# Performance work log

Measured on AMD Instinct MI355X. Metric: run time of the kernel, lower is better.

## Reference

```python
import jax, jax.numpy as jnp
import numpy as np

N = 10000      # atoms
E = 320000     # edges (avg degree 32)
C = 128        # hidden_channels
NB = 32        # num_basis
L = 3          # num_layers
CUT = 5.0      # cutoff
G = 8          # graphs in batch


def setup_inputs() -> dict:
    key = jax.random.key(0)
    ks = jax.random.split(key, 32)
    pos = jax.random.normal(ks[0], (N, 3), dtype=jnp.float32) * 2.0
    z = jax.random.randint(ks[1], (N,), 0, 100)
    row = jax.random.randint(ks[2], (E,), 0, N)
    # avoid self-loops so edge_length > 0
    col = (row + 1 + jax.random.randint(ks[3], (E,), 0, N - 1)) % N
    edge_index = jnp.stack([row, col])
    shifts = jnp.zeros((E, 3), dtype=jnp.float32)
    batch_index = jnp.sort(jax.random.randint(ks[4], (N,), 0, G))
    s = 0.05
    p = lambda k, shape: jax.random.normal(k, shape, dtype=jnp.float32) * s
    return {
        'z': z, 'pos': pos, 'edge_index': edge_index, 'shifts': shifts,
        'batch_index': batch_index,
        'emb': p(ks[5], (100, C)),
        # message blocks (stacked over layers)
        'm_w1': p(ks[6], (L, C, C)), 'm_b1': p(ks[7], (L, C)),
        'm_w2': p(ks[8], (L, C, 3 * C)), 'm_b2': p(ks[9], (L, 3 * C)),
        'f_w': p(ks[10], (L, NB, 3 * C)), 'f_b': p(ks[11], (L, 3 * C)),
        # update blocks
        'u_w': p(ks[12], (L, C, C)), 'v_w': p(ks[13], (L, C, C)),
        'up_w1': p(ks[14], (L, 2 * C, C)), 'up_b1': p(ks[15], (L, C)),
        'up_w2': p(ks[16], (L, C, 3 * C)), 'up_b2': p(ks[17], (L, 3 * C)),
        # readout
        'r_w1': p(ks[18], (C, C // 2)), 'r_b1': p(ks[19], (C // 2,)),
        'r_w2': p(ks[20], (C // 2, 1)), 'r_b2': p(ks[21], (1,)),
    }


def painn_energy(pos, shifts, emb, m_w1, m_b1, m_w2, m_b2, f_w, f_b,
                 u_w, v_w, up_w1, up_b1, up_w2, up_b2,
                 r_w1, r_b1, r_w2, r_b2, z, edge_index, batch_index):
    row, col = edge_index[0], edge_index[1]
    scalar = emb[z]                                  # [N, C]
    vector = jnp.zeros((N, 3, C), dtype=pos.dtype)   # [N, 3, C]

    edge_vec = pos[col] - pos[row] + shifts          # [E, 3]
    edge_len = jnp.sqrt(jnp.sum(edge_vec * edge_vec, axis=-1) + 1e-12)  # [E]
    direction = edge_vec / edge_len[:, None]

    # smooth bump envelope (C-inf, compact support)
    scaled = edge_len / CUT
    inside = scaled < 1.0
    denom = jnp.where(inside, 1.0 - scaled * scaled, 1.0)
    gate = jnp.where(inside, jnp.exp(1.0 - 1.0 / denom), 0.0)  # [E]

    # gaussian radial basis
    centers = jnp.linspace(0.0, CUT, NB)
    gamma = 1.0 / (centers[1] - centers[0]) ** 2
    rbf = jnp.exp(-gamma * (edge_len[:, None] - centers) ** 2)  # [E, NB]
    edge_attr = rbf * gate[:, None]

    for l in range(L):
        # --- message ---
        h = jax.nn.silu(scalar[col] @ m_w1[l] + m_b1[l]) @ m_w2[l] + m_b2[l]  # [E, 3C]
        w = h * (edge_attr @ f_w[l] + f_b[l]) * gate[:, None]
        w1, w2, w3 = jnp.split(w, 3, axis=-1)                                 # each [E, C]
        d_scalar = jax.ops.segment_sum(w1, row, num_segments=N)
        msg_vec = vector[col] * w2[:, None, :] + w3[:, None, :] * direction[:, :, None]  # [E,3,C]
        d_vector = jax.ops.segment_sum(msg_vec, row, num_segments=N)
        scalar = scalar + d_scalar
        vector = vector + d_vector
        # --- update ---
        uv = vector @ u_w[l]                                   # [N, 3, C]
        vv = vector @ v_w[l]
        v_norm = jnp.sqrt(jnp.sum(vv * vv, axis=1) + 1e-8)     # [N, C]
        a = jax.nn.silu(jnp.concatenate([scalar, v_norm], axis=-1) @ up_w1[l] + up_b1[l]) @ up_w2[l] + up_b2[l]
        a1, a2, a3 = jnp.split(a, 3, axis=-1)
        scalar = scalar + a1 + a2 * jnp.sum(uv * vv, axis=1)
        vector = vector + a3[:, None, :] * uv

    e_atom = jax.nn.silu(scalar @ r_w1 + r_b1) @ r_w2 + r_b2   # [N, 1]
    return jax.ops.segment_sum(e_atom, batch_index, num_segments=G)  # [G, 1]


def reference(z, pos, edge_index, shifts, batch_index, emb,
              m_w1, m_b1, m_w2, m_b2, f_w, f_b,
              u_w, v_w, up_w1, up_b1, up_w2, up_b2,
              r_w1, r_b1, r_w2, r_b2):
    return painn_energy(pos, shifts, emb, m_w1, m_b1, m_w2, m_b2, f_w, f_b,
                        u_w, v_w, up_w1, up_b1, up_w2, up_b2,
                        r_w1, r_b1, r_w2, r_b2, z, edge_index, batch_index)
```

## Files before the change

kernel.cpp:

```cpp
#include <hip/hip_runtime.h>
#include <math.h>

#define CUTR 5.0f
#define TL 2048
#define NBASIS 32
#define HSC 16.0f
#define TSC 16.0f
#define VSC 64.0f
#define INV_HT (1.0f / (HSC * TSC))
#define INV_HTV (1.0f / (HSC * TSC * VSC))

typedef __attribute__((ext_vector_type(8))) short bf16x8;
typedef __attribute__((ext_vector_type(4))) float f32x4;
typedef __attribute__((ext_vector_type(2))) float f32x2;

struct U3 { uint x, y, z; };
struct U2 { uint x, y; };

__device__ __forceinline__ float silu_f(float x) { return x / (1.0f + expf(-x)); }
__device__ __forceinline__ ushort f2bf(float x) {
  uint b = __float_as_uint(x);
  uint r = (b + 0x7FFFu + ((b >> 16) & 1u)) >> 16;
  return (ushort)r;
}
__device__ __forceinline__ float bf2f(ushort u) { return __uint_as_float((uint)u << 16); }
__device__ __forceinline__ uchar f2fp8(float x) {
  return (uchar)(__builtin_amdgcn_cvt_pk_fp8_f32(x, 0.0f, 0, false) & 0xff);
}
__device__ __forceinline__ f32x2 fp8lo(uint u) {
  return __builtin_amdgcn_cvt_pk_f32_fp8((int)u, false);
}
__device__ __forceinline__ f32x2 fp8hi(uint u) {
  return __builtin_amdgcn_cvt_pk_f32_fp8((int)u, true);
}

__global__ __launch_bounds__(384) void table_kernel(const float* __restrict__ f_w,
                                                    const float* __restrict__ f_b,
                                                    uchar* __restrict__ tab) {
  __shared__ float fws[NBASIS * 384];
  __shared__ float rbf[8][NBASIS];
  __shared__ float gv[8];
  int tid = threadIdx.x;
  int bi = blockIdx.x;
  int l = bi >> 8, tb = bi & 255;
  for (int i = tid; i < NBASIS * 384; i += 384) fws[i] = f_w[l * NBASIS * 384 + i];
  if (tid < 256) {
    int tt = tid >> 5, k = tid & 31;
    float len = (float)(tb * 8 + tt) * (CUTR / (float)(TL - 1));
    const float gamma = (31.0f / 5.0f) * (31.0f / 5.0f);
    float c = 5.0f * (float)k / 31.0f;
    float d = len - c;
    rbf[tt][k] = expf(-gamma * d * d);
    if (k == 0) {
      float s = len * (1.0f / CUTR);
      gv[tt] = (s < 1.0f) ? expf(1.0f - 1.0f / (1.0f - s * s)) : 0.0f;
    }
  }
  __syncthreads();
  int j = tid % 384;
  int b = j >> 7, ch = j & 127;
  float fb = f_b[l * 384 + j];
  for (int tt = 0; tt < 8; ++tt) {
    float acc = 0.0f;
#pragma unroll
    for (int k = 0; k < NBASIS; ++k) acc += rbf[tt][k] * fws[k * 384 + j];
    float g = gv[tt];
    tab[((size_t)l * TL + (size_t)(tb * 8 + tt)) * 512 + (ch >> 1) * 8 + b * 2 + (ch & 1)] =
        f2fp8(g * (g * acc + fb) * TSC);
  }
}

__global__ __launch_bounds__(256) void init_kernel(
    const int* __restrict__ z, const float* __restrict__ emb, float* __restrict__ scalar,
    ushort* __restrict__ sbf, const float* __restrict__ m_w1, const float* __restrict__ m_w2,
    const float* __restrict__ u_w, const float* __restrict__ v_w,
    const float* __restrict__ up_w1, const float* __restrict__ up_w2,
    const float* __restrict__ r_w1, ushort* __restrict__ wt, const float* __restrict__ pos,
    const int* __restrict__ ei, const float* __restrict__ shifts, int* __restrict__ counts,
    int N, int E) {
  int tid = threadIdx.x;
  int bi = blockIdx.x;
  int nbEmb = (N * 128 + 255) / 256;
  int nbW = (548864 + 255) / 256;
  if (bi < nbEmb) {
    int idx = bi * 256 + tid;
    if (idx >= N * 128) return;
    int n = idx >> 7, j = idx & 127;
    float v = emb[z[n] * 128 + j];
    scalar[idx] = v;
    sbf[idx] = f2bf(v);
    return;
  }
  bi -= nbEmb;
  if (bi < nbW) {
    int idx = bi * 256 + tid;
    if (idx >= 548864) return;
    float v;
    if (idx >= 540672) {
      int t = idx - 540672;
      int n = t >> 7, k = t & 127;
      v = r_w1[k * 64 + n];
    } else {
      int l = idx / 180224, local = idx % 180224;
      if (local < 16384) {
        int n = local >> 7, k = local & 127;
        v = m_w1[l * 16384 + k * 128 + n];
      } else if (local < 65536) {
        int t = local - 16384;
        int n = t >> 7, k = t & 127;
        v = m_w2[l * 49152 + k * 384 + n];
      } else if (local < 98304) {
        int t = local - 65536;
        int n = t >> 7, k = t & 127;
        v = (n < 128) ? u_w[l * 16384 + k * 128 + n] : v_w[l * 16384 + k * 128 + (n - 128)];
      } else if (local < 131072) {
        int t = local - 98304;
        int n = t >> 8, k = t & 255;
        v = up_w1[l * 32768 + k * 128 + n];
      } else {
        int t = local - 131072;
        int n = t >> 7, k = t & 127;
        v = up_w2[l * 49152 + k * 384 + n];
      }
    }
    wt[idx] = f2bf(v);
    return;
  }
  bi -= nbW;
  {
    int e = bi * 256 + tid;
    if (e >= E) return;
    int r = ei[e], c = ei[E + e];
    float dx = pos[c * 3 + 0] - pos[r * 3 + 0] + shifts[e * 3 + 0];
    float dy = pos[c * 3 + 1] - pos[r * 3 + 1] + shifts[e * 3 + 1];
    float dz = pos[c * 3 + 2] - pos[r * 3 + 2] + shifts[e * 3 + 2];
    float len = sqrtf(dx * dx + dy * dy + dz * dz + 1e-12f);
    if (len < CUTR) atomicAdd(&counts[r], 1);
  }
}

__global__ __launch_bounds__(1024) void scan_kernel(const int* __restrict__ counts,
                                                    int* __restrict__ offs,
                                                    int* __restrict__ cursor, int N) {
  __shared__ int sm[1024];
  int tid = threadIdx.x;
  int CH = (N + 1023) / 1024;
  int base = tid * CH;
  int sum = 0;
  for (int i = 0; i < CH; i++) sum += (base + i < N) ? counts[base + i] : 0;
  sm[tid] = sum;
  __syncthreads();
  for (int o = 1; o < 1024; o <<= 1) {
    int v = (tid >= o) ? sm[tid - o] : 0;
    __syncthreads();
    sm[tid] += v;
    __syncthreads();
  }
  int run = sm[tid] - sum;
  for (int i = 0; i < CH; i++) {
    if (base + i < N) {
      offs[base + i] = run;
      cursor[base + i] = run;
      run += counts[base + i];
    }
  }
  if (tid == 1023) offs[N] = sm[1023];
}

__global__ void fill_kernel(const float* __restrict__ pos, const int* __restrict__ ei,
                            const float* __restrict__ shifts, int* __restrict__ cursor,
                            float4* __restrict__ pk, int E) {
  int e = blockIdx.x * 256 + threadIdx.x;
  if (e >= E) return;
  int r = ei[e], c = ei[E + e];
  float dx = pos[c * 3 + 0] - pos[r * 3 + 0] + shifts[e * 3 + 0];
  float dy = pos[c * 3 + 1] - pos[r * 3 + 1] + shifts[e * 3 + 1];
  float dz = pos[c * 3 + 2] - pos[r * 3 + 2] + shifts[e * 3 + 2];
  float len = sqrtf(dx * dx + dy * dy + dz * dz + 1e-12f);
  if (len >= CUTR) return;
  float inv = 1.0f / len;
  float x = len * ((float)(TL - 1) / CUTR);
  int ib = (int)(x + 0.5f);
  if (ib > TL - 1) ib = TL - 1;
  int p = atomicAdd(&cursor[r], 1);
  pk[p] = make_float4(__int_as_float(c | (ib << 14)), dx * inv, dy * inv, dz * inv);
}

template <bool FIRST>
__global__ __launch_bounds__(256) void message_kernel(
    const int* __restrict__ offs, const float4* __restrict__ pk, const uchar* __restrict__ hv8,
    const uchar* __restrict__ tab8, float* __restrict__ scalar, ushort* __restrict__ sbf,
    float* __restrict__ vec, ushort* __restrict__ vbout, int N) {
  int lane = threadIdx.x & 63;
  int n = blockIdx.x * 4 + (threadIdx.x >> 6);
  if (n >= N) return;
  int p0 = offs[n], p1 = offs[n + 1];
  float aS0 = 0.f, aS1 = 0.f;
  float aW00 = 0.f, aW01 = 0.f, aW10 = 0.f, aW11 = 0.f, aW20 = 0.f, aW21 = 0.f;
  float aD00 = 0.f, aD01 = 0.f, aD10 = 0.f, aD11 = 0.f, aD20 = 0.f, aD21 = 0.f;
  int p = p0;
  bool hasA = p < p1, hasB = p + 1 < p1;
  float4 cA, cB;
  if (hasA) cA = pk[p];
  if (hasB) cB = pk[p + 1];
  while (hasA) {
    int bitsA = __float_as_int(cA.x);
    int colA = bitsA & 16383, ibA = bitsA >> 14;
    U3 hvA;
    if (FIRST) {
      U2 t = *(const U2*)(hv8 + (size_t)colA * 768 + lane * 12);
      hvA.x = t.x; hvA.y = t.y; hvA.z = 0;
    } else {
      hvA = *(const U3*)(hv8 + (size_t)colA * 768 + lane * 12);
    }
    U2 tA = *(const U2*)(tab8 + (size_t)ibA * 512 + lane * 8);
    U3 hvB;
    U2 tB;
    float4 dB;
    if (hasB) {
      int bitsB = __float_as_int(cB.x);
      int colB = bitsB & 16383, ibB = bitsB >> 14;
      dB = cB;
      if (FIRST) {
        U2 t = *(const U2*)(hv8 + (size_t)colB * 768 + lane * 12);
        hvB.x = t.x; hvB.y = t.y; hvB.z = 0;
      } else {
        hvB = *(const U3*)(hv8 + (size_t)colB * 768 + lane * 12);
      }
      tB = *(const U2*)(tab8 + (size_t)ibB * 512 + lane * 8);
    }
    int pn = p + 2;
    bool nA = pn < p1, nB = pn + 1 < p1;
    float4 fA, fB;
    if (nA) fA = pk[pn];
    if (nB) fB = pk[pn + 1];
    {
      f32x2 h1 = fp8lo(hvA.x), h2 = fp8hi(hvA.x);
      f32x2 h3 = fp8lo(hvA.y);
      f32x2 t1 = fp8lo(tA.x), t2 = fp8hi(tA.x), t3 = fp8lo(tA.y);
      aS0 += h1.x * t1.x;
      aS1 += h1.y * t1.y;
      float w3l = h3.x * t3.x, w3h = h3.y * t3.y;
      if (!FIRST) {
        f32x2 v0 = fp8hi(hvA.y), v1 = fp8lo(hvA.z), v2 = fp8hi(hvA.z);
        float w2l = h2.x * t2.x, w2h = h2.y * t2.y;
        aW00 += v0.x * w2l; aW01 += v0.y * w2h;
        aW10 += v1.x * w2l; aW11 += v1.y * w2h;
        aW20 += v2.x * w2l; aW21 += v2.y * w2h;
      }
      aD00 += w3l * cA.y; aD01 += w3h * cA.y;
      aD10 += w3l * cA.z; aD11 += w3h * cA.z;
      aD20 += w3l * cA.w; aD21 += w3h * cA.w;
    }
    if (hasB) {
      f32x2 h1 = fp8lo(hvB.x), h2 = fp8hi(hvB.x);
      f32x2 h3 = fp8lo(hvB.y);
      f32x2 t1 = fp8lo(tB.x), t2 = fp8hi(tB.x), t3 = fp8lo(tB.y);
      aS0 += h1.x * t1.x;
      aS1 += h1.y * t1.y;
      float w3l = h3.x * t3.x, w3h = h3.y * t3.y;
      if (!FIRST) {
        f32x2 v0 = fp8hi(hvB.y), v1 = fp8lo(hvB.z), v2 = fp8hi(hvB.z);
        float w2l = h2.x * t2.x, w2h = h2.y * t2.y;
        aW00 += v0.x * w2l; aW01 += v0.y * w2h;
        aW10 += v1.x * w2l; aW11 += v1.y * w2h;
        aW20 += v2.x * w2l; aW21 += v2.y * w2h;
      }
      aD00 += w3l * dB.y; aD01 += w3h * dB.y;
      aD10 += w3l * dB.z; aD11 += w3h * dB.z;
      aD20 += w3l * dB.w; aD21 += w3h * dB.w;
    }
    cA = fA;
    cB = fB;
    hasA = nA;
    hasB = nB;
    p = pn;
  }
  float sS0 = aS0 * INV_HT, sS1 = aS1 * INV_HT;
  float sV00 = aD00 * INV_HT, sV01 = aD01 * INV_HT;
  float sV10 = aD10 * INV_HT, sV11 = aD11 * INV_HT;
  float sV20 = aD20 * INV_HT, sV21 = aD21 * INV_HT;
  if (!FIRST) {
    sV00 += aW00 * INV_HTV; sV01 += aW01 * INV_HTV;
    sV10 += aW10 * INV_HTV; sV11 += aW11 * INV_HTV;
    sV20 += aW20 * INV_HTV; sV21 += aW21 * INV_HTV;
  }
  float2* sp = (float2*)(scalar + (size_t)n * 128) + lane;
  float2 sv = *sp;
  sv.x += sS0;
  sv.y += sS1;
  *sp = sv;
  ((uint*)(sbf + (size_t)n * 128))[lane] = (uint)f2bf(sv.x) | ((uint)f2bf(sv.y) << 16);
  float2* vp0 = (float2*)(vec + (size_t)n * 384) + lane;
  float2* vp1 = (float2*)(vec + (size_t)n * 384 + 128) + lane;
  float2* vp2 = (float2*)(vec + (size_t)n * 384 + 256) + lane;
  float2 v0, v1, v2;
  if (FIRST) {
    v0 = make_float2(sV00, sV01);
    v1 = make_float2(sV10, sV11);
    v2 = make_float2(sV20, sV21);
  } else {
    v0 = *vp0; v1 = *vp1; v2 = *vp2;
    v0.x += sV00; v0.y += sV01;
    v1.x += sV10; v1.y += sV11;
    v2.x += sV20; v2.y += sV21;
  }
  *vp0 = v0; *vp1 = v1; *vp2 = v2;
  uint* ob = (uint*)(vbout + (size_t)n * 384);
  ob[lane] = (uint)f2bf(v0.x) | ((uint)f2bf(v0.y) << 16);
  ob[lane + 64] = (uint)f2bf(v1.x) | ((uint)f2bf(v1.y) << 16);
  ob[lane + 128] = (uint)f2bf(v2.x) | ((uint)f2bf(v2.y) << 16);
}

__global__ __launch_bounds__(512) void mlp_kernel(const ushort* __restrict__ A,
                                                  const ushort* __restrict__ W1T,
                                                  const float* __restrict__ b1,
                                                  const ushort* __restrict__ W2T,
                                                  const float* __restrict__ b2,
                                                  uchar* __restrict__ out, int M) {
  __shared__ ushort As[32 * 128];
  __shared__ ushort Bs[128 * 128];
  __shared__ ushort Hs[32 * 128];
  int tid = threadIdx.x;
  int lane = tid & 63, w = tid >> 6;
  int mh = w >> 2, wc = w & 3;
  int m0 = blockIdx.x * 32;
  int cl = lane & 15, rq = lane >> 4;
  int ra = mh * 16 + cl;
  f32x4 acc[2] = {};
  {
    {
      int row = tid >> 4, ch = tid & 15;
      uint4 av = make_uint4(0, 0, 0, 0);
      if (m0 + row < M) av = *(const uint4*)(A + (size_t)(m0 + row) * 128 + ch * 8);
      *(uint4*)(&As[row * 128 + ((ch ^ (row & 7)) * 8)]) = av;
    }
#pragma unroll
    for (int r = 0; r < 4; ++r) {
      int c = tid + r * 512;
      int row = c >> 4, ch = c & 15;
      uint4 bv = *(const uint4*)(W1T + (size_t)row * 128 + ch * 8);
      *(uint4*)(&Bs[row * 128 + ((ch ^ (row & 7)) * 8)]) = bv;
    }
    __syncthreads();
#pragma unroll
    for (int ks = 0; ks < 4; ++ks) {
      int ch = ks * 4 + rq;
      bf16x8 a = *(bf16x8*)&As[ra * 128 + ((ch ^ (ra & 7)) * 8)];
#pragma unroll
      for (int ns = 0; ns < 2; ++ns) {
        int rb = wc * 32 + ns * 16 + cl;
        bf16x8 b = *(bf16x8*)&Bs[rb * 128 + ((ch ^ (rb & 7)) * 8)];
        acc[ns] = __builtin_amdgcn_mfma_f32_16x16x32_bf16(a, b, acc[ns], 0, 0, 0);
      }
    }
  }
#pragma unroll
  for (int ns = 0; ns < 2; ++ns) {
    int hcol = wc * 32 + ns * 16 + cl;
    float bv = b1[hcol];
    int chunk = hcol >> 3, el = hcol & 7;
#pragma unroll
    for (int j = 0; j < 4; ++j) {
      int hr = mh * 16 + rq * 4 + j;
      float v = silu_f(acc[ns][j] + bv);
      Hs[hr * 128 + ((chunk ^ (hr & 7)) * 8) + el] = f2bf(v);
    }
  }
  __syncthreads();
  for (int nt = 0; nt < 3; ++nt) {
#pragma unroll
    for (int r = 0; r < 4; ++r) {
      int c = tid + r * 512;
      int row = c >> 4, ch = c & 15;
      uint4 bv = *(const uint4*)(W2T + (size_t)(nt * 128 + row) * 128 + ch * 8);
      *(uint4*)(&Bs[row * 128 + ((ch ^ (row & 7)) * 8)]) = bv;
    }
    __syncthreads();
    f32x4 acc2[2] = {};
#pragma unroll
    for (int ks = 0; ks < 4; ++ks) {
      int ch = ks * 4 + rq;
      bf16x8 a = *(bf16x8*)&Hs[ra * 128 + ((ch ^ (ra & 7)) * 8)];
#pragma unroll
      for (int ns = 0; ns < 2; ++ns) {
        int rb = wc * 32 + ns * 16 + cl;
        bf16x8 b = *(bf16x8*)&Bs[rb * 128 + ((ch ^ (rb & 7)) * 8)];
        acc2[ns] = __builtin_amdgcn_mfma_f32_16x16x32_bf16(a, b, acc2[ns], 0, 0, 0);
      }
    }
#pragma unroll
    for (int ns = 0; ns < 2; ++ns) {
      int ch = wc * 32 + ns * 16 + cl;
      float bv = b2[nt * 128 + ch];
#pragma unroll
      for (int j = 0; j < 4; ++j) {
        int m = m0 + mh * 16 + rq * 4 + j;
        if (m >= M) continue;
        out[(size_t)m * 768 + (ch >> 1) * 12 + nt * 2 + (ch & 1)] =
            f2fp8((acc2[ns][j] + bv) * HSC);
      }
    }
    __syncthreads();
  }
}

template <bool LAST>
__global__ __launch_bounds__(512) void mlp2_kernel(
    const ushort* __restrict__ sbf_in, const ushort* __restrict__ W1T,
    const float* __restrict__ b1, const ushort* __restrict__ W2T, const float* __restrict__ b2,
    const ushort* __restrict__ uvvv, float* __restrict__ scalar, ushort* __restrict__ sbf,
    float* __restrict__ vec, uchar* __restrict__ hv8, const ushort* __restrict__ W1nT,
    const float* __restrict__ b1n, const ushort* __restrict__ W2nT,
    const float* __restrict__ b2n, int M) {
  __shared__ ushort As[16 * 128];
  __shared__ ushort Bs[128 * 128];
  __shared__ ushort Hs[16 * 128];
  int tid = threadIdx.x;
  int lane = tid & 63, w = tid >> 6;
  int m0 = blockIdx.x * 16;
  int cl = lane & 15, rq = lane >> 4;
  int rb = w * 16 + cl;
  f32x4 acc = {};
  for (int k0 = 0; k0 < 256; k0 += 128) {
    __syncthreads();
    if (tid < 256) {
      int row = tid >> 4, ch = tid & 15;
      uint4 av = make_uint4(0, 0, 0, 0);
      if (m0 + row < M) {
        if (k0 == 0) {
          av = *(const uint4*)(sbf_in + (size_t)(m0 + row) * 128 + ch * 8);
        } else {
          const ushort* ub = uvvv + (size_t)(m0 + row) * 768 + 128 + ch * 8;
          bf16x8 x0 = *(const bf16x8*)(ub);
          bf16x8 x1 = *(const bf16x8*)(ub + 256);
          bf16x8 x2 = *(const bf16x8*)(ub + 512);
          ushort pkv[8];
#pragma unroll
          for (int e = 0; e < 8; ++e) {
            float a = bf2f((ushort)x0[e]), bb = bf2f((ushort)x1[e]), cc = bf2f((ushort)x2[e]);
            pkv[e] = f2bf(sqrtf(a * a + bb * bb + cc * cc + 1e-8f));
          }
          av = *(uint4*)pkv;
        }
      }
      *(uint4*)(&As[row * 128 + ((ch ^ (row & 7)) * 8)]) = av;
    }
#pragma unroll
    for (int r = 0; r < 4; ++r) {
      int c = tid + r * 512;
      int row = c >> 4, ch = c & 15;
      uint4 bv = *(const uint4*)(W1T + (size_t)row * 256 + k0 + ch * 8);
      *(uint4*)(&Bs[row * 128 + ((ch ^ (row & 7)) * 8)]) = bv;
    }
    __syncthreads();
#pragma unroll
    for (int ks = 0; ks < 4; ++ks) {
      int ch = ks * 4 + rq;
      bf16x8 a = *(bf16x8*)&As[cl * 128 + ((ch ^ (cl & 7)) * 8)];
      bf16x8 b = *(bf16x8*)&Bs[rb * 128 + ((ch ^ (rb & 7)) * 8)];
      acc = __builtin_amdgcn_mfma_f32_16x16x32_bf16(a, b, acc, 0, 0, 0);
    }
  }
  {
    int hcol = w * 16 + cl;
    float bv = b1[hcol];
    int chunk = hcol >> 3, el = hcol & 7;
#pragma unroll
    for (int j = 0; j < 4; ++j) {
      int hr = rq * 4 + j;
      Hs[hr * 128 + ((chunk ^ (hr & 7)) * 8) + el] = f2bf(silu_f(acc[j] + bv));
    }
  }
  __syncthreads();
  f32x4 aReg[3];
  for (int nt = 0; nt < 3; ++nt) {
#pragma unroll
    for (int r = 0; r < 4; ++r) {
      int c = tid + r * 512;
      int row = c >> 4, ch = c & 15;
      uint4 bv = *(const uint4*)(W2T + (size_t)(nt * 128 + row) * 128 + ch * 8);
      *(uint4*)(&Bs[row * 128 + ((ch ^ (row & 7)) * 8)]) = bv;
    }
    __syncthreads();
    f32x4 acc2 = {};
#pragma unroll
    for (int ks = 0; ks < 4; ++ks) {
      int ch = ks * 4 + rq;
      bf16x8 a = *(bf16x8*)&Hs[cl * 128 + ((ch ^ (cl & 7)) * 8)];
      bf16x8 b = *(bf16x8*)&Bs[rb * 128 + ((ch ^ (rb & 7)) * 8)];
      acc2 = __builtin_amdgcn_mfma_f32_16x16x32_bf16(a, b, acc2, 0, 0, 0);
    }
    aReg[nt] = acc2;
    __syncthreads();
  }
  {
    int chOff = w * 16 + cl;
    float b2a = b2[chOff], b2b = b2[128 + chOff], b2c = b2[256 + chOff];
#pragma unroll
    for (int j = 0; j < 4; ++j) {
      int nn = m0 + rq * 4 + j;
      if (nn >= M) continue;
      float a1 = aReg[0][j] + b2a;
      float a2 = aReg[1][j] + b2b;
      float a3 = aReg[2][j] + b2c;
      const ushort* ub = uvvv + (size_t)nn * 768;
      float uv0 = bf2f(ub[chOff]), vv0 = bf2f(ub[128 + chOff]);
      float uv1 = bf2f(ub[256 + chOff]), vv1 = bf2f(ub[384 + chOff]);
      float uv2 = bf2f(ub[512 + chOff]), vv2 = bf2f(ub[640 + chOff]);
      float dot = uv0 * vv0 + uv1 * vv1 + uv2 * vv2;
      size_t si = (size_t)nn * 128 + chOff;
      float s = scalar[si] + a1 + a2 * dot;
      scalar[si] = s;
      ushort sb = f2bf(s);
      sbf[si] = sb;
      if (!LAST) {
        int lr = rq * 4 + j;
        As[lr * 128 + (((chOff >> 3) ^ (lr & 7)) * 8) + (chOff & 7)] = sb;
        size_t vb = (size_t)nn * 384 + chOff;
        float nv0 = vec[vb] + a3 * uv0;
        float nv1 = vec[vb + 128] + a3 * uv1;
        float nv2 = vec[vb + 256] + a3 * uv2;
        vec[vb] = nv0;
        vec[vb + 128] = nv1;
        vec[vb + 256] = nv2;
        size_t hb = (size_t)nn * 768 + (chOff >> 1) * 12 + 6 + (chOff & 1);
        hv8[hb] = f2fp8(nv0 * VSC);
        hv8[hb + 2] = f2fp8(nv1 * VSC);
        hv8[hb + 4] = f2fp8(nv2 * VSC);
      }
    }
  }
  if (LAST) return;
#pragma unroll
  for (int r = 0; r < 4; ++r) {
    int c = tid + r * 512;
    int row = c >> 4, ch = c & 15;
    uint4 bv = *(const uint4*)(W1nT + (size_t)row * 128 + ch * 8);
    *(uint4*)(&Bs[row * 128 + ((ch ^ (row & 7)) * 8)]) = bv;
  }
  __syncthreads();
  f32x4 acc3 = {};
#pragma unroll
  for (int ks = 0; ks < 4; ++ks) {
    int ch = ks * 4 + rq;
    bf16x8 a = *(bf16x8*)&As[cl * 128 + ((ch ^ (cl & 7)) * 8)];
    bf16x8 b = *(bf16x8*)&Bs[rb * 128 + ((ch ^ (rb & 7)) * 8)];
    acc3 = __builtin_amdgcn_mfma_f32_16x16x32_bf16(a, b, acc3, 0, 0, 0);
  }
  __syncthreads();
  {
    int hcol = w * 16 + cl;
    float bv = b1n[hcol];
    int chunk = hcol >> 3, el = hcol & 7;
#pragma unroll
    for (int j = 0; j < 4; ++j) {
      int hr = rq * 4 + j;
      Hs[hr * 128 + ((chunk ^ (hr & 7)) * 8) + el] = f2bf(silu_f(acc3[j] + bv));
    }
  }
  __syncthreads();
  for (int nt = 0; nt < 3; ++nt) {
#pragma unroll
    for (int r = 0; r < 4; ++r) {
      int c = tid + r * 512;
      int row = c >> 4, ch = c & 15;
      uint4 bv = *(const uint4*)(W2nT + (size_t)(nt * 128 + row) * 128 + ch * 8);
      *(uint4*)(&Bs[row * 128 + ((ch ^ (row & 7)) * 8)]) = bv;
    }
    __syncthreads();
    f32x4 acc4 = {};
#pragma unroll
    for (int ks = 0; ks < 4; ++ks) {
      int ch = ks * 4 + rq;
      bf16x8 a = *(bf16x8*)&Hs[cl * 128 + ((ch ^ (cl & 7)) * 8)];
      bf16x8 b = *(bf16x8*)&Bs[rb * 128 + ((ch ^ (rb & 7)) * 8)];
      acc4 = __builtin_amdgcn_mfma_f32_16x16x32_bf16(a, b, acc4, 0, 0, 0);
    }
    {
      int ch = w * 16 + cl;
      float bv = b2n[nt * 128 + ch];
#pragma unroll
      for (int j = 0; j < 4; ++j) {
        int m = m0 + rq * 4 + j;
        if (m >= M) continue;
        hv8[(size_t)m * 768 + (ch >> 1) * 12 + nt * 2 + (ch & 1)] =
            f2fp8((acc4[j] + bv) * HSC);
      }
    }
    __syncthreads();
  }
}

__global__ __launch_bounds__(256) void gemm_kernel(const ushort* __restrict__ A,
                                                   const ushort* __restrict__ WT,
                                                   ushort* __restrict__ Cout, int M, int K,
                                                   int Nn) {
  __shared__ ushort As[64 * 128];
  __shared__ ushort Bs[64 * 128];
  int tid = threadIdx.x;
  int m0 = blockIdx.x * 64, n0 = blockIdx.y * 64;
  int lane = tid & 63, w = tid >> 6, wr = w >> 1, wc = w & 1;
  f32x4 acc[2][2] = {};
  for (int k0 = 0; k0 < K; k0 += 128) {
    __syncthreads();
#pragma unroll
    for (int r = 0; r < 4; ++r) {
      int c = tid + r * 256;
      int row = c >> 4, col16 = c & 15;
      uint4 av = make_uint4(0, 0, 0, 0);
      if (m0 + row < M) av = *(const uint4*)(A + (size_t)(m0 + row) * K + k0 + col16 * 8);
      *(uint4*)(&As[row * 128 + ((col16 ^ (row & 7)) * 8)]) = av;
      uint4 bv = *(const uint4*)(WT + (size_t)(n0 + row) * K + k0 + col16 * 8);
      *(uint4*)(&Bs[row * 128 + ((col16 ^ (row & 7)) * 8)]) = bv;
    }
    __syncthreads();
#pragma unroll
    for (int ks = 0; ks < 4; ++ks) {
      int ch = ks * 4 + (lane >> 4);
      int ra0 = wr * 32 + (lane & 15), ra1 = ra0 + 16;
      int rb0 = wc * 32 + (lane & 15), rb1 = rb0 + 16;
      bf16x8 a0 = *(bf16x8*)&As[ra0 * 128 + ((ch ^ (ra0 & 7)) * 8)];
      bf16x8 a1 = *(bf16x8*)&As[ra1 * 128 + ((ch ^ (ra1 & 7)) * 8)];
      bf16x8 b0 = *(bf16x8*)&Bs[rb0 * 128 + ((ch ^ (rb0 & 7)) * 8)];
      bf16x8 b1 = *(bf16x8*)&Bs[rb1 * 128 + ((ch ^ (rb1 & 7)) * 8)];
      acc[0][0] = __builtin_amdgcn_mfma_f32_16x16x32_bf16(a0, b0, acc[0][0], 0, 0, 0);
      acc[0][1] = __builtin_amdgcn_mfma_f32_16x16x32_bf16(a0, b1, acc[0][1], 0, 0, 0);
      acc[1][0] = __builtin_amdgcn_mfma_f32_16x16x32_bf16(a1, b0, acc[1][0], 0, 0, 0);
      acc[1][1] = __builtin_amdgcn_mfma_f32_16x16x32_bf16(a1, b1, acc[1][1], 0, 0, 0);
    }
  }
  int cl = lane & 15, rq = lane >> 4;
#pragma unroll
  for (int ms = 0; ms < 2; ++ms)
#pragma unroll
    for (int ns = 0; ns < 2; ++ns) {
      int n = n0 + wc * 32 + ns * 16 + cl;
#pragma unroll
      for (int j = 0; j < 4; ++j) {
        int m = m0 + wr * 32 + ms * 16 + rq * 4 + j;
        if (m >= M) continue;
        Cout[(size_t)m * Nn + n] = f2bf(acc[ms][ns][j]);
      }
    }
}

__global__ __launch_bounds__(256) void readout_kernel(
    const ushort* __restrict__ sbf, const ushort* __restrict__ r1T, const float* __restrict__ rb1,
    const float* __restrict__ r_w2, const float* __restrict__ r_b2, const int* __restrict__ bidx,
    float* __restrict__ out, int N, int G) {
  __shared__ ushort As[64 * 128];
  __shared__ ushort Bs[64 * 128];
  __shared__ float rs[64];
  __shared__ float sm[64];
  int tid = threadIdx.x;
  int m0 = blockIdx.x * 64;
  int lane = tid & 63, w = tid >> 6, wr = w >> 1, wc = w & 1;
  int cl = lane & 15, rq = lane >> 4;
#pragma unroll
  for (int r = 0; r < 4; ++r) {
    int c = tid + r * 256;
    int row = c >> 4, ch = c & 15;
    uint4 av = make_uint4(0, 0, 0, 0);
    if (m0 + row < N) av = *(const uint4*)(sbf + (size_t)(m0 + row) * 128 + ch * 8);
    *(uint4*)(&As[row * 128 + ((ch ^ (row & 7)) * 8)]) = av;
    uint4 bv = *(const uint4*)(r1T + (size_t)row * 128 + ch * 8);
    *(uint4*)(&Bs[row * 128 + ((ch ^ (row & 7)) * 8)]) = bv;
  }
  if (tid < 64) {
    rs[tid] = 0.f;
    sm[tid] = 0.f;
  }
  __syncthreads();
  f32x4 acc[2][2] = {};
#pragma unroll
  for (int ks = 0; ks < 4; ++ks) {
    int ch = ks * 4 + rq;
    int ra0 = wr * 32 + cl, ra1 = ra0 + 16;
    int rb0 = wc * 32 + cl, rb1 = rb0 + 16;
    bf16x8 a0 = *(bf16x8*)&As[ra0 * 128 + ((ch ^ (ra0 & 7)) * 8)];
    bf16x8 a1 = *(bf16x8*)&As[ra1 * 128 + ((ch ^ (ra1 & 7)) * 8)];
    bf16x8 b0 = *(bf16x8*)&Bs[rb0 * 128 + ((ch ^ (rb0 & 7)) * 8)];
    bf16x8 b1 = *(bf16x8*)&Bs[rb1 * 128 + ((ch ^ (rb1 & 7)) * 8)];
    acc[0][0] = __builtin_amdgcn_mfma_f32_16x16x32_bf16(a0, b0, acc[0][0], 0, 0, 0);
    acc[0][1] = __builtin_amdgcn_mfma_f32_16x16x32_bf16(a0, b1, acc[0][1], 0, 0, 0);
    acc[1][0] = __builtin_amdgcn_mfma_f32_16x16x32_bf16(a1, b0, acc[1][0], 0, 0, 0);
    acc[1][1] = __builtin_amdgcn_mfma_f32_16x16x32_bf16(a1, b1, acc[1][1], 0, 0, 0);
  }
#pragma unroll
  for (int ms = 0; ms < 2; ++ms) {
    float part0 = 0.f, part1 = 0.f, part2 = 0.f, part3 = 0.f;
#pragma unroll
    for (int ns = 0; ns < 2; ++ns) {
      int col = wc * 32 + ns * 16 + cl;
      float b1v = rb1[col], wv = r_w2[col];
      part0 += silu_f(acc[ms][ns][0] + b1v) * wv;
      part1 += silu_f(acc[ms][ns][1] + b1v) * wv;
      part2 += silu_f(acc[ms][ns][2] + b1v) * wv;
      part3 += silu_f(acc[ms][ns][3] + b1v) * wv;
    }
#pragma unroll
    for (int o = 1; o < 16; o <<= 1) {
      part0 += __shfl_xor(part0, o);
      part1 += __shfl_xor(part1, o);
      part2 += __shfl_xor(part2, o);
      part3 += __shfl_xor(part3, o);
    }
    if (cl == 0) {
      int rbase = wr * 32 + ms * 16 + rq * 4;
      atomicAdd(&rs[rbase + 0], part0);
      atomicAdd(&rs[rbase + 1], part1);
      atomicAdd(&rs[rbase + 2], part2);
      atomicAdd(&rs[rbase + 3], part3);
    }
  }
  __syncthreads();
  float rb2 = r_b2[0];
  if (tid < 64) {
    int m = m0 + tid;
    if (m < N) atomicAdd(&sm[bidx[m]], rs[tid] + rb2);
  }
  __syncthreads();
  if (tid < G && G <= 64) atomicAdd(&out[tid], sm[tid]);
}

extern "C" void kernel_launch(void* const* d_in, const int* in_sizes, int n_in, void* d_out,
                              int out_size, void* d_ws, size_t ws_size, hipStream_t stream) {
  const int N = in_sizes[0];
  const int E = in_sizes[2] / 2;
  const int G = out_size;

  const int* z = (const int*)d_in[0];
  const float* pos = (const float*)d_in[1];
  const int* ei = (const int*)d_in[2];
  const float* shifts = (const float*)d_in[3];
  const int* bidx = (const int*)d_in[4];
  const float* emb = (const float*)d_in[5];
  const float* m_w1 = (const float*)d_in[6];
  const float* m_b1 = (const float*)d_in[7];
  const float* m_w2 = (const float*)d_in[8];
  const float* m_b2 = (const float*)d_in[9];
  const float* f_w = (const float*)d_in[10];
  const float* f_b = (const float*)d_in[11];
  const float* u_w = (const float*)d_in[12];
  const float* v_w = (const float*)d_in[13];
  const float* up_w1 = (const float*)d_in[14];
  const float* up_b1 = (const float*)d_in[15];
  const float* up_w2 = (const float*)d_in[16];
  const float* up_b2 = (const float*)d_in[17];
  const float* r_w1 = (const float*)d_in[18];
  const float* r_b1 = (const float*)d_in[19];
  const float* r_w2 = (const float*)d_in[20];
  const float* r_b2 = (const float*)d_in[21];
  float* out = (float*)d_out;

  float* w = (float*)d_ws;
  size_t off = 0;
  auto alloc = [&](size_t nfl) { float* p = w + off; off += (nfl + 3) & ~(size_t)3; return p; };
  uchar* tab8 = (uchar*)alloc((size_t)3 * TL * 128);
  float* scalar = alloc((size_t)N * 128);
  ushort* sbf = (ushort*)alloc((size_t)N * 64);
  float* vec = alloc((size_t)N * 384);
  uchar* hv8 = (uchar*)alloc((size_t)N * 192);
  ushort* mir_bf = (ushort*)alloc((size_t)N * 192);
  ushort* uvvv = (ushort*)alloc((size_t)N * 384);
  float* pkf = alloc((size_t)E * 4);
  ushort* wt = (ushort*)alloc((size_t)274432);
  int* counts = (int*)alloc((size_t)N);
  int* offs = (int*)alloc((size_t)N + 4);
  int* cursor = (int*)alloc((size_t)N);
  if (off * sizeof(float) > ws_size) return;

  hipMemsetAsync(counts, 0, (size_t)N * sizeof(int), stream);
  hipMemsetAsync(out, 0, (size_t)G * sizeof(float), stream);

  table_kernel<<<3 * (TL / 8), 384, 0, stream>>>(f_w, f_b, tab8);
  int nbEmb = (N * 128 + 255) / 256;
  int nbW = (548864 + 255) / 256;
  int nbCount = (E + 255) / 256;
  init_kernel<<<nbEmb + nbW + nbCount, 256, 0, stream>>>(z, emb, scalar, sbf, m_w1, m_w2, u_w,
                                                         v_w, up_w1, up_w2, r_w1, wt, pos, ei,
                                                         shifts, counts, N, E);
  scan_kernel<<<1, 1024, 0, stream>>>(counts, offs, cursor, N);
  fill_kernel<<<(E + 255) / 256, 256, 0, stream>>>(pos, ei, shifts, cursor, (float4*)pkf, E);

  dim3 gm((N + 31) / 32);
  dim3 gm2((N + 15) / 16);
  dim3 g3((3 * N + 63) / 64, 4);

  mlp_kernel<<<gm, 512, 0, stream>>>(sbf, wt, m_b1, wt + 16384, m_b2, hv8, N);

  for (int l = 0; l < 3; l++) {
    const ushort* wl = wt + (size_t)l * 180224;
    if (l == 0)
      message_kernel<true><<<(N + 3) / 4, 256, 0, stream>>>(
          offs, (const float4*)pkf, hv8, tab8 + (size_t)l * TL * 512, scalar, sbf, vec, mir_bf,
          N);
    else
      message_kernel<false><<<(N + 3) / 4, 256, 0, stream>>>(
          offs, (const float4*)pkf, hv8, tab8 + (size_t)l * TL * 512, scalar, sbf, vec, mir_bf,
          N);
    gemm_kernel<<<g3, 256, 0, stream>>>(mir_bf, wl + 65536, uvvv, 3 * N, 128, 256);
    if (l < 2) {
      const ushort* wn = wt + (size_t)(l + 1) * 180224;
      mlp2_kernel<false><<<gm2, 512, 0, stream>>>(
          sbf, wl + 98304, up_b1 + l * 128, wl + 131072, up_b2 + l * 384, uvvv, scalar, sbf, vec,
          hv8, wn, m_b1 + (l + 1) * 128, wn + 16384, m_b2 + (l + 1) * 384, N);
    } else {
      mlp2_kernel<true><<<gm2, 512, 0, stream>>>(
          sbf, wl + 98304, up_b1 + l * 128, wl + 131072, up_b2 + l * 384, uvvv, scalar, sbf, vec,
          hv8, wt, m_b1, wt, m_b2, N);
    }
  }

  readout_kernel<<<(N + 63) / 64, 256, 0, stream>>>(sbf, wt + 540672, r_b1, r_w2, r_b2, bidx,
                                                    out, N, G);
}
```

Before: 305.5 us.

## Prepack MLP weights in MFMA fragment order and read directly from global

Adds a pre-pass in init_kernel that converts the update-MLP and next-layer message-MLP weights into a bf16 layout matching the per-lane MFMA B-fragment order. mlp2_kernel then loads B fragments straight from global or L2 instead of staging 128x128 weight tiles through shared memory. This removes the large Bs buffer and most __syncthreads, which cuts LDS use and may raise occupancy. In exchange every 16-row block re-reads the full weights from cache, and the A operand is now built in registers per lane.

```diff
diff --git a/kernel.cpp b/kernel.cpp
--- a/kernel.cpp
+++ b/kernel.cpp
@@ -75,13 +75,14 @@
     ushort* __restrict__ sbf, const float* __restrict__ m_w1, const float* __restrict__ m_w2,
     const float* __restrict__ u_w, const float* __restrict__ v_w,
     const float* __restrict__ up_w1, const float* __restrict__ up_w2,
-    const float* __restrict__ r_w1, ushort* __restrict__ wt, const float* __restrict__ pos,
-    const int* __restrict__ ei, const float* __restrict__ shifts, int* __restrict__ counts,
-    int N, int E) {
+    const float* __restrict__ r_w1, ushort* __restrict__ wt, ushort* __restrict__ wp,
+    const float* __restrict__ pos, const int* __restrict__ ei, const float* __restrict__ shifts,
+    int* __restrict__ counts, int N, int E) {
   int tid = threadIdx.x;
   int bi = blockIdx.x;
   int nbEmb = (N * 128 + 255) / 256;
   int nbW = (548864 + 255) / 256;
+  int nbP = (442368 + 255) / 256;
   if (bi < nbEmb) {
     int idx = bi * 256 + tid;
     if (idx >= N * 128) return;
@@ -127,6 +128,47 @@
     return;
   }
   bi -= nbW;
+  if (bi < nbP) {
+    int idx = bi * 256 + tid;
+    if (idx >= 442368) return;
+    int l = idx / 147456, loc = idx % 147456;
+    float v;
+    if (loc < 32768) {
+      int fid = loc >> 9, li = loc & 511;
+      int ctg = fid >> 3, f = fid & 7;
+      int lane = li >> 3, e = li & 7;
+      int col = ctg * 16 + (lane & 15);
+      int k = (f * 4 + (lane >> 4)) * 8 + e;
+      v = up_w1[l * 32768 + k * 128 + col];
+    } else if (loc < 81920) {
+      int t = loc - 32768;
+      int fid = t >> 9, li = t & 511;
+      int ctg = fid >> 2, f = fid & 3;
+      int lane = li >> 3, e = li & 7;
+      int col = ctg * 16 + (lane & 15);
+      int k = (f * 4 + (lane >> 4)) * 8 + e;
+      v = up_w2[l * 49152 + k * 384 + col];
+    } else if (loc < 98304) {
+      int t = loc - 81920;
+      int fid = t >> 9, li = t & 511;
+      int ctg = fid >> 2, f = fid & 3;
+      int lane = li >> 3, e = li & 7;
+      int col = ctg * 16 + (lane & 15);
+      int k = (f * 4 + (lane >> 4)) * 8 + e;
+      v = m_w1[l * 16384 + k * 128 + col];
+    } else {
+      int t = loc - 98304;
+      int fid = t >> 9, li = t & 511;
+      int ctg = fid >> 2, f = fid & 3;
+      int lane = li >> 3, e = li & 7;
+      int col = ctg * 16 + (lane & 15);
+      int k = (f * 4 + (lane >> 4)) * 8 + e;
+      v = m_w2[l * 49152 + k * 384 + col];
+    }
+    wp[idx] = f2bf(v);
+    return;
+  }
+  bi -= nbP;
   {
     int e = bi * 256 + tid;
     if (e >= E) return;
@@ -407,60 +449,45 @@
 
 template <bool LAST>
 __global__ __launch_bounds__(512) void mlp2_kernel(
-    const ushort* __restrict__ sbf_in, const ushort* __restrict__ W1T,
-    const float* __restrict__ b1, const ushort* __restrict__ W2T, const float* __restrict__ b2,
+    const ushort* __restrict__ sbf_in, const ushort* __restrict__ p_w1,
+    const float* __restrict__ b1, const ushort* __restrict__ p_w2, const float* __restrict__ b2,
     const ushort* __restrict__ uvvv, float* __restrict__ scalar, ushort* __restrict__ sbf,
-    float* __restrict__ vec, uchar* __restrict__ hv8, const ushort* __restrict__ W1nT,
-    const float* __restrict__ b1n, const ushort* __restrict__ W2nT,
+    float* __restrict__ vec, uchar* __restrict__ hv8, const ushort* __restrict__ p_m1,
+    const float* __restrict__ b1n, const ushort* __restrict__ p_m2,
     const float* __restrict__ b2n, int M) {
-  __shared__ ushort As[16 * 128];
-  __shared__ ushort Bs[128 * 128];
+  __shared__ ushort Ss[16 * 128];
   __shared__ ushort Hs[16 * 128];
   int tid = threadIdx.x;
   int lane = tid & 63, w = tid >> 6;
   int m0 = blockIdx.x * 16;
   int cl = lane & 15, rq = lane >> 4;
-  int rb = w * 16 + cl;
+  int row = m0 + cl;
+  bool rok = row < M;
   f32x4 acc = {};
-  for (int k0 = 0; k0 < 256; k0 += 128) {
-    __syncthreads();
-    if (tid < 256) {
-      int row = tid >> 4, ch = tid & 15;
-      uint4 av = make_uint4(0, 0, 0, 0);
-      if (m0 + row < M) {
-        if (k0 == 0) {
-          av = *(const uint4*)(sbf_in + (size_t)(m0 + row) * 128 + ch * 8);
-        } else {
-          const ushort* ub = uvvv + (size_t)(m0 + row) * 768 + 128 + ch * 8;
-          bf16x8 x0 = *(const bf16x8*)(ub);
-          bf16x8 x1 = *(const bf16x8*)(ub + 256);
-          bf16x8 x2 = *(const bf16x8*)(ub + 512);
-          ushort pkv[8];
-#pragma unroll
-          for (int e = 0; e < 8; ++e) {
-            float a = bf2f((ushort)x0[e]), bb = bf2f((ushort)x1[e]), cc = bf2f((ushort)x2[e]);
-            pkv[e] = f2bf(sqrtf(a * a + bb * bb + cc * cc + 1e-8f));
-          }
-          av = *(uint4*)pkv;
+#pragma unroll
+  for (int f = 0; f < 8; ++f) {
+    int ch = f * 4 + rq;
+    ushort az[8] = {0, 0, 0, 0, 0, 0, 0, 0};
+    bf16x8 a;
+    if (f < 4) {
+      a = rok ? *(const bf16x8*)(sbf_in + (size_t)row * 128 + ch * 8) : *(bf16x8*)az;
+    } else {
+      if (rok) {
+        int j = (ch - 16) * 8;
+        const ushort* ub = uvvv + (size_t)row * 768 + 128 + j;
+        bf16x8 x0 = *(const bf16x8*)(ub);
+        bf16x8 x1 = *(const bf16x8*)(ub + 256);
+        bf16x8 x2 = *(const bf16x8*)(ub + 512);
+#pragma unroll
+        for (int e = 0; e < 8; ++e) {
+          float aa = bf2f((ushort)x0[e]), bb = bf2f((ushort)x1[e]), cc = bf2f((ushort)x2[e]);
+          az[e] = f2bf(sqrtf(aa * aa + bb * bb + cc * cc + 1e-8f));
         }
       }
-      *(uint4*)(&As[row * 128 + ((ch ^ (row & 7)) * 8)]) = av;
-    }
-#pragma unroll
-    for (int r = 0; r < 4; ++r) {
-      int c = tid + r * 512;
-      int row = c >> 4, ch = c & 15;
-      uint4 bv = *(const uint4*)(W1T + (size_t)row * 256 + k0 + ch * 8);
-      *(uint4*)(&Bs[row * 128 + ((ch ^ (row & 7)) * 8)]) = bv;
-    }
-    __syncthreads();
-#pragma unroll
-    for (int ks = 0; ks < 4; ++ks) {
-      int ch = ks * 4 + rq;
-      bf16x8 a = *(bf16x8*)&As[cl * 128 + ((ch ^ (cl & 7)) * 8)];
-      bf16x8 b = *(bf16x8*)&Bs[rb * 128 + ((ch ^ (rb & 7)) * 8)];
-      acc = __builtin_amdgcn_mfma_f32_16x16x32_bf16(a, b, acc, 0, 0, 0);
-    }
+      a = *(bf16x8*)az;
+    }
+    bf16x8 b = *(const bf16x8*)(p_w1 + ((size_t)(w * 8 + f) * 64 + lane) * 8);
+    acc = __builtin_amdgcn_mfma_f32_16x16x32_bf16(a, b, acc, 0, 0, 0);
   }
   {
     int hcol = w * 16 + cl;
@@ -474,25 +501,17 @@
   }
   __syncthreads();
   f32x4 aReg[3];
+#pragma unroll
   for (int nt = 0; nt < 3; ++nt) {
-#pragma unroll
-    for (int r = 0; r < 4; ++r) {
-      int c = tid + r * 512;
-      int row = c >> 4, ch = c & 15;
-      uint4 bv = *(const uint4*)(W2T + (size_t)(nt * 128 + row) * 128 + ch * 8);
-      *(uint4*)(&Bs[row * 128 + ((ch ^ (row & 7)) * 8)]) = bv;
-    }
-    __syncthreads();
     f32x4 acc2 = {};
 #pragma unroll
     for (int ks = 0; ks < 4; ++ks) {
       int ch = ks * 4 + rq;
       bf16x8 a = *(bf16x8*)&Hs[cl * 128 + ((ch ^ (cl & 7)) * 8)];
-      bf16x8 b = *(bf16x8*)&Bs[rb * 128 + ((ch ^ (rb & 7)) * 8)];
+      bf16x8 b = *(const bf16x8*)(p_w2 + ((size_t)((nt * 8 + w) * 4 + ks) * 64 + lane) * 8);
       acc2 = __builtin_amdgcn_mfma_f32_16x16x32_bf16(a, b, acc2, 0, 0, 0);
     }
     aReg[nt] = acc2;
-    __syncthreads();
   }
   {
     int chOff = w * 16 + cl;
@@ -516,7 +535,7 @@
       sbf[si] = sb;
       if (!LAST) {
         int lr = rq * 4 + j;
-        As[lr * 128 + (((chOff >> 3) ^ (lr & 7)) * 8) + (chOff & 7)] = sb;
+        Ss[lr * 128 + (((chOff >> 3) ^ (lr & 7)) * 8) + (chOff & 7)] = sb;
         size_t vb = (size_t)nn * 384 + chOff;
         float nv0 = vec[vb] + a3 * uv0;
         float nv1 = vec[vb + 128] + a3 * uv1;
@@ -532,23 +551,15 @@
     }
   }
   if (LAST) return;
-#pragma unroll
-  for (int r = 0; r < 4; ++r) {
-    int c = tid + r * 512;
-    int row = c >> 4, ch = c & 15;
-    uint4 bv = *(const uint4*)(W1nT + (size_t)row * 128 + ch * 8);
-    *(uint4*)(&Bs[row * 128 + ((ch ^ (row & 7)) * 8)]) = bv;
-  }
   __syncthreads();
   f32x4 acc3 = {};
 #pragma unroll
   for (int ks = 0; ks < 4; ++ks) {
     int ch = ks * 4 + rq;
-    bf16x8 a = *(bf16x8*)&As[cl * 128 + ((ch ^ (cl & 7)) * 8)];
-    bf16x8 b = *(bf16x8*)&Bs[rb * 128 + ((ch ^ (rb & 7)) * 8)];
+    bf16x8 a = *(bf16x8*)&Ss[cl * 128 + ((ch ^ (cl & 7)) * 8)];
+    bf16x8 b = *(const bf16x8*)(p_m1 + ((size_t)(w * 4 + ks) * 64 + lane) * 8);
     acc3 = __builtin_amdgcn_mfma_f32_16x16x32_bf16(a, b, acc3, 0, 0, 0);
   }
-  __syncthreads();
   {
     int hcol = w * 16 + cl;
     float bv = b1n[hcol];
@@ -560,35 +571,24 @@
     }
   }
   __syncthreads();
+#pragma unroll
   for (int nt = 0; nt < 3; ++nt) {
-#pragma unroll
-    for (int r = 0; r < 4; ++r) {
-      int c = tid + r * 512;
-      int row = c >> 4, ch = c & 15;
-      uint4 bv = *(const uint4*)(W2nT + (size_t)(nt * 128 + row) * 128 + ch * 8);
-      *(uint4*)(&Bs[row * 128 + ((ch ^ (row & 7)) * 8)]) = bv;
-    }
-    __syncthreads();
     f32x4 acc4 = {};
 #pragma unroll
     for (int ks = 0; ks < 4; ++ks) {
       int ch = ks * 4 + rq;
       bf16x8 a = *(bf16x8*)&Hs[cl * 128 + ((ch ^ (cl & 7)) * 8)];
-      bf16x8 b = *(bf16x8*)&Bs[rb * 128 + ((ch ^ (rb & 7)) * 8)];
+      bf16x8 b = *(const bf16x8*)(p_m2 + ((size_t)((nt * 8 + w) * 4 + ks) * 64 + lane) * 8);
       acc4 = __builtin_amdgcn_mfma_f32_16x16x32_bf16(a, b, acc4, 0, 0, 0);
     }
-    {
-      int ch = w * 16 + cl;
-      float bv = b2n[nt * 128 + ch];
-#pragma unroll
-      for (int j = 0; j < 4; ++j) {
-        int m = m0 + rq * 4 + j;
-        if (m >= M) continue;
-        hv8[(size_t)m * 768 + (ch >> 1) * 12 + nt * 2 + (ch & 1)] =
-            f2fp8((acc4[j] + bv) * HSC);
-      }
-    }
-    __syncthreads();
+    int ch = w * 16 + cl;
+    float bv = b2n[nt * 128 + ch];
+#pragma unroll
+    for (int j = 0; j < 4; ++j) {
+      int m = m0 + rq * 4 + j;
+      if (m >= M) continue;
+      hv8[(size_t)m * 768 + (ch >> 1) * 12 + nt * 2 + (ch & 1)] = f2fp8((acc4[j] + bv) * HSC);
+    }
   }
 }
 
@@ -766,6 +766,7 @@
   ushort* uvvv = (ushort*)alloc((size_t)N * 384);
   float* pkf = alloc((size_t)E * 4);
   ushort* wt = (ushort*)alloc((size_t)274432);
+  ushort* wp = (ushort*)alloc((size_t)221184);
   int* counts = (int*)alloc((size_t)N);
   int* offs = (int*)alloc((size_t)N + 4);
   int* cursor = (int*)alloc((size_t)N);
@@ -777,10 +778,11 @@
   table_kernel<<<3 * (TL / 8), 384, 0, stream>>>(f_w, f_b, tab8);
   int nbEmb = (N * 128 + 255) / 256;
   int nbW = (548864 + 255) / 256;
+  int nbP = (442368 + 255) / 256;
   int nbCount = (E + 255) / 256;
-  init_kernel<<<nbEmb + nbW + nbCount, 256, 0, stream>>>(z, emb, scalar, sbf, m_w1, m_w2, u_w,
-                                                         v_w, up_w1, up_w2, r_w1, wt, pos, ei,
-                                                         shifts, counts, N, E);
+  init_kernel<<<nbEmb + nbW + nbP + nbCount, 256, 0, stream>>>(
+      z, emb, scalar, sbf, m_w1, m_w2, u_w, v_w, up_w1, up_w2, r_w1, wt, wp, pos, ei, shifts,
+      counts, N, E);
   scan_kernel<<<1, 1024, 0, stream>>>(counts, offs, cursor, N);
   fill_kernel<<<(E + 255) / 256, 256, 0, stream>>>(pos, ei, shifts, cursor, (float4*)pkf, E);
 
@@ -792,6 +794,7 @@
 
   for (int l = 0; l < 3; l++) {
     const ushort* wl = wt + (size_t)l * 180224;
+    const ushort* pl = wp + (size_t)l * 147456;
     if (l == 0)
       message_kernel<true><<<(N + 3) / 4, 256, 0, stream>>>(
           offs, (const float4*)pkf, hv8, tab8 + (size_t)l * TL * 512, scalar, sbf, vec, mir_bf,
@@ -802,14 +805,14 @@
           N);
     gemm_kernel<<<g3, 256, 0, stream>>>(mir_bf, wl + 65536, uvvv, 3 * N, 128, 256);
     if (l < 2) {
-      const ushort* wn = wt + (size_t)(l + 1) * 180224;
+      const ushort* pn = wp + (size_t)(l + 1) * 147456;
       mlp2_kernel<false><<<gm2, 512, 0, stream>>>(
-          sbf, wl + 98304, up_b1 + l * 128, wl + 131072, up_b2 + l * 384, uvvv, scalar, sbf, vec,
-          hv8, wn, m_b1 + (l + 1) * 128, wn + 16384, m_b2 + (l + 1) * 384, N);
+          sbf, pl, up_b1 + l * 128, pl + 32768, up_b2 + l * 384, uvvv, scalar, sbf, vec, hv8,
+          pn + 81920, m_b1 + (l + 1) * 128, pn + 98304, m_b2 + (l + 1) * 384, N);
     } else {
       mlp2_kernel<true><<<gm2, 512, 0, stream>>>(
-          sbf, wl + 98304, up_b1 + l * 128, wl + 131072, up_b2 + l * 384, uvvv, scalar, sbf, vec,
-          hv8, wt, m_b1, wt, m_b2, N);
+          sbf, pl, up_b1 + l * 128, pl + 32768, up_b2 + l * 384, uvvv, scalar, sbf, vec, hv8,
+          pl, m_b1, pl, m_b2, N);
     }
   }
 
```

Measured after the change: 319.9 us. 4.7% more time.
